# Kernel tuning notes

Measured on AMD Instinct MI355X. Metric: run time of the kernel, lower is better.

Reference implementation:

```python
import jax, jax.numpy as jnp
import numpy as np

V, E, H, B, T = 32000, 256, 512, 16, 256


def setup_inputs() -> dict:
    key = jax.random.key(0)
    ks = jax.random.split(key, 12)
    s = 1.0 / np.sqrt(H)  # torch nn.RNN init range
    u = lambda k, shape: jax.random.uniform(k, shape, jnp.float32, -s, s)
    return dict(
        X=jax.random.randint(ks[0], (B, T), 0, V),
        emb=jax.random.normal(ks[1], (V, E), jnp.float32),
        W_ih0=u(ks[2], (H, E)), W_hh0=u(ks[3], (H, H)),
        b_ih0=u(ks[4], (H,)), b_hh0=u(ks[5], (H,)),
        W_ih1=u(ks[6], (H, H)), W_hh1=u(ks[7], (H, H)),
        b_ih1=u(ks[8], (H,)), b_hh1=u(ks[9], (H,)),
        W_fc=u(ks[10], (V, H)), b_fc=u(ks[11], (V,)),
    )


def _rnn_layer(x, W_ih, W_hh, b_ih, b_hh):
    """Elman RNN layer, batch_first. x: [B,T,D] -> (outputs [B,T,H], h_T [B,H]).
    h_t = tanh(x_t @ W_ih^T + b_ih + h_{t-1} @ W_hh^T + b_hh), h_0 = 0."""
    # Precompute the input projection for all timesteps (one big GEMM).
    xp = jnp.einsum('btd,hd->bth', x, W_ih) + b_ih + b_hh  # [B,T,H]

    def step(h, xt):
        h = jnp.tanh(xt + h @ W_hh.T)
        return h, h

    h0 = jnp.zeros((x.shape[0], W_hh.shape[0]), x.dtype)
    hT, ys = jax.lax.scan(step, h0, jnp.swapaxes(xp, 0, 1))  # scan over T
    return jnp.swapaxes(ys, 0, 1), hT


def reference(X, emb, W_ih0, W_hh0, b_ih0, b_hh0,
              W_ih1, W_hh1, b_ih1, b_hh1, W_fc, b_fc):
    x = emb[X]  # [B,T,E]
    out1, h1 = _rnn_layer(x, W_ih0, W_hh0, b_ih0, b_hh0)
    out2, h2 = _rnn_layer(out1, W_ih1, W_hh1, b_ih1, b_hh1)
    logits = jnp.einsum('bth,vh->btv', out2, W_fc) + b_fc  # [B,T,V]
    hidden = jnp.stack([h1, h2], axis=0)  # [n_layers, B, H]
    return logits, hidden, out2
```

## Files before the change

kernel.cpp:

```cpp
#include <hip/hip_runtime.h>
#include <hip/hip_fp16.h>

#define BB 16
#define TT 256
#define HH 512
#define EE 256
#define VV 32000

using half8   = __attribute__((ext_vector_type(8))) _Float16;
using float4v = __attribute__((ext_vector_type(4))) float;
typedef unsigned long long u64;

#define WS_WFC16   0u
#define WS_XG      32768000u
#define WS_WIH0    34865152u
#define WS_WIH1    35127296u
#define WS_XP0     35651584u
#define WS_XP1     44040192u
#define WS_H0EX    52428800u
#define WS_OUT2F16 56623104u
#define WS_FLAGS   60817408u
#define WS_NEEDED  60833792u

__global__ void init_flags_k(unsigned* f) {
    f[blockIdx.x * 256 + threadIdx.x] = 0u;
}

__global__ void cvt_f32_f16_k(const float* __restrict__ s, _Float16* __restrict__ d, int n) {
    int i = blockIdx.x * 256 + threadIdx.x;
    if (i < n) d[i] = (_Float16)s[i];
}

__global__ void gather_embed_k(const int* __restrict__ X, const float* __restrict__ emb,
                               _Float16* __restrict__ xg) {
    int m = blockIdx.x;
    int e = threadIdx.x;
    int row = X[m];
    xg[m * EE + e] = (_Float16)emb[(size_t)row * EE + e];
}

template <bool PERM>
__global__ __launch_bounds__(256)
void gemm_f16_k(const _Float16* __restrict__ A, const _Float16* __restrict__ Bm,
                const float* __restrict__ bias0, const float* __restrict__ bias1,
                float* __restrict__ C, int M, int N, int K) {
    __shared__ _Float16 As[128][40];
    __shared__ _Float16 Bs[128][40];
    const int tid = threadIdx.x;
    const int l = tid & 63, w = tid >> 6;
    const int ntiles = N >> 7;
    const int m0 = (blockIdx.x / ntiles) << 7;
    const int n0 = (blockIdx.x % ntiles) << 7;
    const int wr = (w >> 1) << 6, wc = (w & 1) << 6;
    const int lrow = tid >> 1, lseg = (tid & 1) << 4;
    const int ar = l & 15, ak = (l >> 4) << 3;

    float4v acc[4][4] = {};

    for (int kt = 0; kt < K; kt += 32) {
        const _Float16* ga = A  + (size_t)(m0 + lrow) * K + kt + lseg;
        const _Float16* gb = Bm + (size_t)(n0 + lrow) * K + kt + lseg;
        *(int4*)&As[lrow][lseg]     = *(const int4*)ga;
        *(int4*)&As[lrow][lseg + 8] = *(const int4*)(ga + 8);
        *(int4*)&Bs[lrow][lseg]     = *(const int4*)gb;
        *(int4*)&Bs[lrow][lseg + 8] = *(const int4*)(gb + 8);
        __syncthreads();

        half8 af[4], bf[4];
#pragma unroll
        for (int m = 0; m < 4; ++m) af[m] = *(half8*)&As[wr + m * 16 + ar][ak];
#pragma unroll
        for (int n = 0; n < 4; ++n) bf[n] = *(half8*)&Bs[wc + n * 16 + ar][ak];
#pragma unroll
        for (int m = 0; m < 4; ++m)
#pragma unroll
            for (int n = 0; n < 4; ++n)
                acc[m][n] = __builtin_amdgcn_mfma_f32_16x16x32_f16(af[m], bf[n], acc[m][n], 0, 0, 0);
        __syncthreads();
    }

#pragma unroll
    for (int m = 0; m < 4; ++m) {
#pragma unroll
        for (int n = 0; n < 4; ++n) {
            const int col = n0 + wc + n * 16 + (l & 15);
            float bv = (bias0 ? bias0[col] : 0.f) + (bias1 ? bias1[col] : 0.f);
#pragma unroll
            for (int r = 0; r < 4; ++r) {
                const int row = m0 + wr + m * 16 + ((l >> 4) << 2) + r;
                float v = acc[m][n][r] + bv;
                if (PERM) {
                    int t = row & 255, b = row >> 8;
                    C[(size_t)((t << 4) + b) * HH + col] = v;
                } else {
                    C[(size_t)row * N + col] = v;
                }
            }
        }
    }
}

__device__ __forceinline__ float tanh_fast(float x) {
    float e = __expf(2.0f * x);
    return 1.0f - 2.0f * __builtin_amdgcn_rcpf(e + 1.0f);
}

__global__ __launch_bounds__(512, 2)
void rnn_pipe_k(const float* __restrict__ Whh0, const float* __restrict__ Whh1,
                const _Float16* __restrict__ Wih1f16,
                const float* __restrict__ bih1, const float* __restrict__ bhh1,
                const float* __restrict__ xp0, float* __restrict__ xp1,
                unsigned* __restrict__ h0ex,
                _Float16* __restrict__ out2f16, float* __restrict__ out_hidden,
                float* __restrict__ out2f32,
                unsigned* __restrict__ flags0, unsigned* __restrict__ flag1x)
{
    __shared__ _Float16 hbuf[16][520];
    __shared__ _Float16 wlds[8 * 4 * 4 * 64 * 8];

    const int tid = threadIdx.x;
    const int l = tid & 63, w = tid >> 6;
    const int lq = l >> 4;
    const int kq = lq << 3;
    const int c15 = l & 15;
    const int bi = blockIdx.x;

    if (bi < 2) {
        const int layer = bi;
        const float* Whh = layer ? Whh1 : Whh0;

        half8 wf[4][12];
#pragma unroll
        for (int ct = 0; ct < 4; ++ct) {
            const int col = w * 64 + ct * 16 + c15;
            const float* wrow = Whh + (size_t)col * HH;
#pragma unroll
            for (int kt = 0; kt < 16; ++kt) {
                const float* s = wrow + kt * 32 + kq;
                float4v f0 = *(const float4v*)s;
                float4v f1 = *(const float4v*)(s + 4);
                half8 h;
#pragma unroll
                for (int i = 0; i < 4; ++i) { h[i] = (_Float16)f0[i]; h[i + 4] = (_Float16)f1[i]; }
                if (kt < 12) wf[ct][kt] = h;
                else *(half8*)&wlds[((((w * 4 + ct) * 4) + (kt - 12)) * 64 + l) * 8] = h;
            }
        }

        float4v acc[4], accn[4];
        if (layer == 0) {
#pragma unroll
            for (int ct = 0; ct < 4; ++ct) {
                const int col = w * 64 + ct * 16 + c15;
#pragma unroll
                for (int r = 0; r < 4; ++r)
                    acc[ct][r] = xp0[(size_t)(lq * 4 + r) * HH + col];
            }
        } else {
            while (!__hip_atomic_load(&flag1x[0], __ATOMIC_ACQUIRE, __HIP_MEMORY_SCOPE_AGENT))
                __builtin_amdgcn_s_sleep(2);
#pragma unroll
            for (int ct = 0; ct < 4; ++ct) {
                const int col = w * 64 + ct * 16 + c15;
#pragma unroll
                for (int r = 0; r < 4; ++r)
                    acc[ct][r] = __hip_atomic_load(&xp1[(size_t)(lq * 4 + r) * HH + col],
                                                   __ATOMIC_RELAXED, __HIP_MEMORY_SCOPE_AGENT);
            }
        }
        __syncthreads();

        for (int t = 0; t < TT; ++t) {
            if (t > 0) {
#pragma unroll
                for (int kt = 0; kt < 16; ++kt) {
                    half8 a = *(const half8*)&hbuf[c15][kt * 32 + kq];
                    half8 b0, b1, b2, b3;
                    if (kt < 12) {
                        b0 = wf[0][kt]; b1 = wf[1][kt]; b2 = wf[2][kt]; b3 = wf[3][kt];
                    } else {
                        b0 = *(const half8*)&wlds[((((w * 4 + 0) * 4) + (kt - 12)) * 64 + l) * 8];
                        b1 = *(const half8*)&wlds[((((w * 4 + 1) * 4) + (kt - 12)) * 64 + l) * 8];
                        b2 = *(const half8*)&wlds[((((w * 4 + 2) * 4) + (kt - 12)) * 64 + l) * 8];
                        b3 = *(const half8*)&wlds[((((w * 4 + 3) * 4) + (kt - 12)) * 64 + l) * 8];
                    }
                    acc[0] = __builtin_amdgcn_mfma_f32_16x16x32_f16(a, b0, acc[0], 0, 0, 0);
                    acc[1] = __builtin_amdgcn_mfma_f32_16x16x32_f16(a, b1, acc[1], 0, 0, 0);
                    acc[2] = __builtin_amdgcn_mfma_f32_16x16x32_f16(a, b2, acc[2], 0, 0, 0);
                    acc[3] = __builtin_amdgcn_mfma_f32_16x16x32_f16(a, b3, acc[3], 0, 0, 0);
                }
            }

            if (layer == 0 && t > 0) {
                asm volatile("s_waitcnt vmcnt(0)" ::: "memory");
                if (l == 0)
                    __hip_atomic_store(&flags0[(t - 1) * 8 + w], 1u,
                                       __ATOMIC_RELAXED, __HIP_MEMORY_SCOPE_AGENT);
            }

            if (t + 1 < TT) {
                if (layer == 0) {
#pragma unroll
                    for (int ct = 0; ct < 4; ++ct) {
                        const int col = w * 64 + ct * 16 + c15;
#pragma unroll
                        for (int r = 0; r < 4; ++r)
                            accn[ct][r] = xp0[(size_t)((t + 1) * 16 + lq * 4 + r) * HH + col];
                    }
                } else {
                    while (!__hip_atomic_load(&flag1x[t + 1], __ATOMIC_ACQUIRE, __HIP_MEMORY_SCOPE_AGENT))
                        __builtin_amdgcn_s_sleep(2);
#pragma unroll
                    for (int ct = 0; ct < 4; ++ct) {
                        const int col = w * 64 + ct * 16 + c15;
#pragma unroll
                        for (int r = 0; r < 4; ++r)
                            accn[ct][r] = __hip_atomic_load(&xp1[(size_t)((t + 1) * 16 + lq * 4 + r) * HH + col],
                                                            __ATOMIC_RELAXED, __HIP_MEMORY_SCOPE_AGENT);
                    }
                }
            }

            unsigned pk[4][4];
#pragma unroll
            for (int ct = 0; ct < 4; ++ct) {
                const int col = w * 64 + ct * 16 + c15;
#pragma unroll
                for (int r = 0; r < 4; ++r) {
                    const int b = lq * 4 + r;
                    float hv = tanh_fast(acc[ct][r]);
                    if (layer)
                        out2f32[((size_t)(b << 8) + t) * HH + col] = hv;
                    if (t == TT - 1)
                        out_hidden[(size_t)(layer * BB + b) * HH + col] = hv;
                    unsigned short mu = __builtin_bit_cast(unsigned short, (_Float16)hv);
                    int ov = __shfl_xor((int)mu, 1, 64);
                    pk[ct][r] = (unsigned)mu | ((unsigned)ov << 16);
                }
            }

            if (layer == 0) {
                unsigned* dst = h0ex + (size_t)t * 4096;
#pragma unroll
                for (int ct = 0; ct < 4; ++ct) {
                    const int col = w * 64 + ct * 16 + c15;
#pragma unroll
                    for (int r = 0; r < 4; ++r)
                        if ((l & 1) == 0)
                            __hip_atomic_store(&dst[(lq * 4 + r) * 256 + (col >> 1)], pk[ct][r],
                                               __ATOMIC_RELAXED, __HIP_MEMORY_SCOPE_AGENT);
                }
            } else {
#pragma unroll
                for (int ct = 0; ct < 4; ++ct) {
                    const int col = w * 64 + ct * 16 + c15;
#pragma unroll
                    for (int r = 0; r < 4; ++r)
                        if ((l & 1) == 0)
                            *(unsigned*)&out2f16[((size_t)((lq * 4 + r) << 8) + t) * HH + col] = pk[ct][r];
                }
            }

            asm volatile("" ::: "memory");
            __builtin_amdgcn_s_barrier();
            asm volatile("" ::: "memory");

#pragma unroll
            for (int ct = 0; ct < 4; ++ct) {
                const int col = w * 64 + ct * 16 + c15;
#pragma unroll
                for (int r = 0; r < 4; ++r)
                    if ((l & 1) == 0)
                        *(unsigned*)&hbuf[lq * 4 + r][col] = pk[ct][r];
            }
            asm volatile("s_waitcnt lgkmcnt(0)" ::: "memory");
            __builtin_amdgcn_s_barrier();
            asm volatile("" ::: "memory");

            if (t + 1 < TT) {
#pragma unroll
                for (int ct = 0; ct < 4; ++ct) acc[ct] = accn[ct];
            }
        }

        if (layer == 0) {
            asm volatile("s_waitcnt vmcnt(0)" ::: "memory");
            if (l == 0)
                __hip_atomic_store(&flags0[(TT - 1) * 8 + w], 1u,
                                   __ATOMIC_RELAXED, __HIP_MEMORY_SCOPE_AGENT);
        }
    } else {
        const int stripe = bi - 2;
        float bsum[4];
#pragma unroll
        for (int ct = 0; ct < 4; ++ct) {
            const int col = w * 64 + ct * 16 + c15;
            bsum[ct] = bih1[col] + bhh1[col];
        }
        const int base64 = c15 * 128 + lq * 2;

        for (int j = 0; j < 8; ++j) {
            const int t = stripe + 32 * j;
            for (;;) {
                unsigned v = 1u;
                if (l < 8)
                    v = __hip_atomic_load(&flags0[t * 8 + l], __ATOMIC_ACQUIRE, __HIP_MEMORY_SCOPE_AGENT);
                if (__all(v != 0)) break;
                __builtin_amdgcn_s_sleep(2);
            }
            half8 af[16];
            const u64* pA = (const u64*)h0ex + (size_t)t * 2048;
#pragma unroll
            for (int kt = 0; kt < 16; ++kt) {
                u64 d0 = __hip_atomic_load(pA + base64 + kt * 8,     __ATOMIC_RELAXED, __HIP_MEMORY_SCOPE_AGENT);
                u64 d1 = __hip_atomic_load(pA + base64 + kt * 8 + 1, __ATOMIC_RELAXED, __HIP_MEMORY_SCOPE_AGENT);
                union { u64 u[2]; half8 h; } cv;
                cv.u[0] = d0; cv.u[1] = d1;
                af[kt] = cv.h;
            }
            float4v acc[4];
#pragma unroll
            for (int ct = 0; ct < 4; ++ct) {
                acc[ct][0] = bsum[ct]; acc[ct][1] = bsum[ct];
                acc[ct][2] = bsum[ct]; acc[ct][3] = bsum[ct];
            }
#pragma unroll
            for (int ct = 0; ct < 4; ++ct) {
                const int col = w * 64 + ct * 16 + c15;
                const _Float16* wp = Wih1f16 + (size_t)col * HH + kq;
#pragma unroll
                for (int kt = 0; kt < 16; ++kt) {
                    half8 bf = *(const half8*)(wp + kt * 32);
                    acc[ct] = __builtin_amdgcn_mfma_f32_16x16x32_f16(af[kt], bf, acc[ct], 0, 0, 0);
                }
            }
#pragma unroll
            for (int ct = 0; ct < 4; ++ct) {
                const int col = w * 64 + ct * 16 + c15;
#pragma unroll
                for (int r = 0; r < 4; ++r)
                    __hip_atomic_store(&xp1[(size_t)(t * 16 + lq * 4 + r) * HH + col], acc[ct][r],
                                       __ATOMIC_RELAXED, __HIP_MEMORY_SCOPE_AGENT);
            }
            __syncthreads();
            if (tid == 0)
                __hip_atomic_store(&flag1x[t], 1u, __ATOMIC_RELEASE, __HIP_MEMORY_SCOPE_AGENT);
        }
    }
}

extern "C" void kernel_launch(void* const* d_in, const int* in_sizes, int n_in,
                              void* d_out, int out_size, void* d_ws, size_t ws_size,
                              hipStream_t stream) {
    if (ws_size < WS_NEEDED) return;

    const int*   X     = (const int*)d_in[0];
    const float* emb   = (const float*)d_in[1];
    const float* Wih0  = (const float*)d_in[2];
    const float* Whh0  = (const float*)d_in[3];
    const float* bih0  = (const float*)d_in[4];
    const float* bhh0  = (const float*)d_in[5];
    const float* Wih1  = (const float*)d_in[6];
    const float* Whh1  = (const float*)d_in[7];
    const float* bih1  = (const float*)d_in[8];
    const float* bhh1  = (const float*)d_in[9];
    const float* Wfc   = (const float*)d_in[10];
    const float* bfc   = (const float*)d_in[11];

    char* ws = (char*)d_ws;
    _Float16* Wfc16   = (_Float16*)(ws + WS_WFC16);
    _Float16* xg      = (_Float16*)(ws + WS_XG);
    _Float16* Wih0f16 = (_Float16*)(ws + WS_WIH0);
    _Float16* Wih1f16 = (_Float16*)(ws + WS_WIH1);
    float*    xp0     = (float*)(ws + WS_XP0);
    float*    xp1     = (float*)(ws + WS_XP1);
    unsigned* h0ex    = (unsigned*)(ws + WS_H0EX);
    _Float16* o2f16   = (_Float16*)(ws + WS_OUT2F16);
    unsigned* flags0  = (unsigned*)(ws + WS_FLAGS);
    unsigned* flag1x  = flags0 + TT * 8;

    float* logits     = (float*)d_out;
    float* hidden     = (float*)d_out + (size_t)BB * TT * VV;
    float* out2       = hidden + 2 * BB * HH;

    hipLaunchKernelGGL(init_flags_k, dim3(9), dim3(256), 0, stream, flags0);
    hipLaunchKernelGGL(gather_embed_k, dim3(BB * TT), dim3(256), 0, stream, X, emb, xg);
    hipLaunchKernelGGL(cvt_f32_f16_k, dim3((HH * EE) / 256), dim3(256), 0, stream, Wih0, Wih0f16, HH * EE);
    hipLaunchKernelGGL(cvt_f32_f16_k, dim3((HH * HH) / 256), dim3(256), 0, stream, Wih1, Wih1f16, HH * HH);
    hipLaunchKernelGGL(cvt_f32_f16_k, dim3((VV * HH) / 256), dim3(256), 0, stream, Wfc, Wfc16, VV * HH);

    hipLaunchKernelGGL((gemm_f16_k<true>), dim3((4096 / 128) * (HH / 128)), dim3(256), 0, stream,
                       xg, Wih0f16, bih0, bhh0, xp0, 4096, HH, EE);

    hipLaunchKernelGGL(rnn_pipe_k, dim3(34), dim3(512), 0, stream,
                       Whh0, Whh1, Wih1f16, bih1, bhh1, xp0, xp1,
                       h0ex, o2f16, hidden, out2, flags0, flag1x);

    hipLaunchKernelGGL((gemm_f16_k<false>), dim3((4096 / 128) * (VV / 128)), dim3(256), 0, stream,
                       o2f16, Wfc16, bfc, nullptr, logits, 4096, VV, HH);
}
```

Baseline: 1.989 ms.

## Halve recurrent block to 4 waves with 128 columns each, restructure step pipeline

Cuts the recurrent blocks from 8 to 4 wavefronts, so each wave owns 128 hidden columns. That doubles the register-held W_hh fragments and the per-wave MFMA count, while the LDS-resident part shrinks to 4 k-tiles. The input projection is no longer prefetched into a second accumulator; it is loaded mid-step between the two MFMA halves and added before tanh. Layer 1 peeks its flag at the start of the step and only spins after the first MFMAs. The aim is to cut barrier and sync overhead per timestep and hide load latency behind the matmul, at the cost of more register pressure and fewer waves sharing the serial step.

Result: slower. 2.361 ms (+18.7%).

```diff
diff --git a/kernel.cpp b/kernel.cpp
--- a/kernel.cpp
+++ b/kernel.cpp
@@ -105,7 +105,7 @@
     return 1.0f - 2.0f * __builtin_amdgcn_rcpf(e + 1.0f);
 }
 
-__global__ __launch_bounds__(512, 2)
+__global__ __launch_bounds__(256, 1)
 void rnn_pipe_k(const float* __restrict__ Whh0, const float* __restrict__ Whh1,
                 const _Float16* __restrict__ Wih1f16,
                 const float* __restrict__ bih1, const float* __restrict__ bhh1,
@@ -116,7 +116,7 @@
                 unsigned* __restrict__ flags0, unsigned* __restrict__ flag1x)
 {
     __shared__ _Float16 hbuf[16][520];
-    __shared__ _Float16 wlds[8 * 4 * 4 * 64 * 8];
+    __shared__ _Float16 wlds[4 * 8 * 4 * 64 * 8];
 
     const int tid = threadIdx.x;
     const int l = tid & 63, w = tid >> 6;
@@ -129,10 +129,10 @@
         const int layer = bi;
         const float* Whh = layer ? Whh1 : Whh0;
 
-        half8 wf[4][12];
-#pragma unroll
-        for (int ct = 0; ct < 4; ++ct) {
-            const int col = w * 64 + ct * 16 + c15;
+        half8 wf[8][12];
+#pragma unroll
+        for (int ct = 0; ct < 8; ++ct) {
+            const int col = w * 128 + ct * 16 + c15;
             const float* wrow = Whh + (size_t)col * HH;
 #pragma unroll
             for (int kt = 0; kt < 16; ++kt) {
@@ -142,93 +142,92 @@
                 half8 h;
 #pragma unroll
                 for (int i = 0; i < 4; ++i) { h[i] = (_Float16)f0[i]; h[i + 4] = (_Float16)f1[i]; }
-                if (kt < 12) wf[ct][kt] = h;
-                else *(half8*)&wlds[((((w * 4 + ct) * 4) + (kt - 12)) * 64 + l) * 8] = h;
-            }
-        }
-
-        float4v acc[4], accn[4];
-        if (layer == 0) {
-#pragma unroll
-            for (int ct = 0; ct < 4; ++ct) {
-                const int col = w * 64 + ct * 16 + c15;
-#pragma unroll
-                for (int r = 0; r < 4; ++r)
-                    acc[ct][r] = xp0[(size_t)(lq * 4 + r) * HH + col];
-            }
-        } else {
-            while (!__hip_atomic_load(&flag1x[0], __ATOMIC_ACQUIRE, __HIP_MEMORY_SCOPE_AGENT))
-                __builtin_amdgcn_s_sleep(2);
-#pragma unroll
-            for (int ct = 0; ct < 4; ++ct) {
-                const int col = w * 64 + ct * 16 + c15;
-#pragma unroll
-                for (int r = 0; r < 4; ++r)
-                    acc[ct][r] = __hip_atomic_load(&xp1[(size_t)(lq * 4 + r) * HH + col],
-                                                   __ATOMIC_RELAXED, __HIP_MEMORY_SCOPE_AGENT);
+                if (kt < 4) *(half8*)&wlds[((((w * 8 + ct) * 4) + kt) * 64 + l) * 8] = h;
+                else wf[ct][kt - 4] = h;
             }
         }
         __syncthreads();
 
+        float4v acc[8] = {};
         for (int t = 0; t < TT; ++t) {
+            unsigned fpre = 1u;
+            if (layer == 0) {
+                if (t > 0) {
+                    asm volatile("s_waitcnt vmcnt(0)" ::: "memory");
+                    if (l == 0)
+                        __hip_atomic_store(&flags0[(t - 1) * 4 + w], 1u,
+                                           __ATOMIC_RELAXED, __HIP_MEMORY_SCOPE_AGENT);
+                }
+            } else {
+                fpre = __hip_atomic_load(&flag1x[t], __ATOMIC_RELAXED, __HIP_MEMORY_SCOPE_AGENT);
+            }
+
             if (t > 0) {
 #pragma unroll
-                for (int kt = 0; kt < 16; ++kt) {
+                for (int kt = 0; kt < 4; ++kt) {
                     half8 a = *(const half8*)&hbuf[c15][kt * 32 + kq];
-                    half8 b0, b1, b2, b3;
-                    if (kt < 12) {
-                        b0 = wf[0][kt]; b1 = wf[1][kt]; b2 = wf[2][kt]; b3 = wf[3][kt];
-                    } else {
-                        b0 = *(const half8*)&wlds[((((w * 4 + 0) * 4) + (kt - 12)) * 64 + l) * 8];
-                        b1 = *(const half8*)&wlds[((((w * 4 + 1) * 4) + (kt - 12)) * 64 + l) * 8];
-                        b2 = *(const half8*)&wlds[((((w * 4 + 2) * 4) + (kt - 12)) * 64 + l) * 8];
-                        b3 = *(const half8*)&wlds[((((w * 4 + 3) * 4) + (kt - 12)) * 64 + l) * 8];
+#pragma unroll
+                    for (int ct = 0; ct < 8; ++ct) {
+                        half8 b = *(const half8*)&wlds[((((w * 8 + ct) * 4) + kt) * 64 + l) * 8];
+                        acc[ct] = __builtin_amdgcn_mfma_f32_16x16x32_f16(a, b, acc[ct], 0, 0, 0);
                     }
-                    acc[0] = __builtin_amdgcn_mfma_f32_16x16x32_f16(a, b0, acc[0], 0, 0, 0);
-                    acc[1] = __builtin_amdgcn_mfma_f32_16x16x32_f16(a, b1, acc[1], 0, 0, 0);
-                    acc[2] = __builtin_amdgcn_mfma_f32_16x16x32_f16(a, b2, acc[2], 0, 0, 0);
-                    acc[3] = __builtin_amdgcn_mfma_f32_16x16x32_f16(a, b3, acc[3], 0, 0, 0);
-                }
-            }
-
-            if (layer == 0 && t > 0) {
-                asm volatile("s_waitcnt vmcnt(0)" ::: "memory");
-                if (l == 0)
-                    __hip_atomic_store(&flags0[(t - 1) * 8 + w], 1u,
-                                       __ATOMIC_RELAXED, __HIP_MEMORY_SCOPE_AGENT);
-            }
-
-            if (t + 1 < TT) {
-                if (layer == 0) {
-#pragma unroll
-                    for (int ct = 0; ct < 4; ++ct) {
-                        const int col = w * 64 + ct * 16 + c15;
-#pragma unroll
-                        for (int r = 0; r < 4; ++r)
-                            accn[ct][r] = xp0[(size_t)((t + 1) * 16 + lq * 4 + r) * HH + col];
-                    }
+                }
+#pragma unroll
+                for (int kt = 4; kt < 8; ++kt) {
+                    half8 a = *(const half8*)&hbuf[c15][kt * 32 + kq];
+#pragma unroll
+                    for (int ct = 0; ct < 8; ++ct)
+                        acc[ct] = __builtin_amdgcn_mfma_f32_16x16x32_f16(a, wf[ct][kt - 4], acc[ct], 0, 0, 0);
+                }
+            }
+
+            if (layer == 1) {
+                if (fpre) {
+                    __builtin_amdgcn_fence(__ATOMIC_ACQUIRE, "agent");
                 } else {
-                    while (!__hip_atomic_load(&flag1x[t + 1], __ATOMIC_ACQUIRE, __HIP_MEMORY_SCOPE_AGENT))
+                    while (!__hip_atomic_load(&flag1x[t], __ATOMIC_ACQUIRE, __HIP_MEMORY_SCOPE_AGENT))
                         __builtin_amdgcn_s_sleep(2);
-#pragma unroll
-                    for (int ct = 0; ct < 4; ++ct) {
-                        const int col = w * 64 + ct * 16 + c15;
-#pragma unroll
-                        for (int r = 0; r < 4; ++r)
-                            accn[ct][r] = __hip_atomic_load(&xp1[(size_t)((t + 1) * 16 + lq * 4 + r) * HH + col],
-                                                            __ATOMIC_RELAXED, __HIP_MEMORY_SCOPE_AGENT);
-                    }
-                }
-            }
-
-            unsigned pk[4][4];
-#pragma unroll
-            for (int ct = 0; ct < 4; ++ct) {
-                const int col = w * 64 + ct * 16 + c15;
+                }
+            }
+
+            float xv[8][4];
+            if (layer == 0) {
+#pragma unroll
+                for (int ct = 0; ct < 8; ++ct) {
+                    const int col = w * 128 + ct * 16 + c15;
+#pragma unroll
+                    for (int r = 0; r < 4; ++r)
+                        xv[ct][r] = xp0[(size_t)(t * 16 + lq * 4 + r) * HH + col];
+                }
+            } else {
+#pragma unroll
+                for (int ct = 0; ct < 8; ++ct) {
+                    const int col = w * 128 + ct * 16 + c15;
+#pragma unroll
+                    for (int r = 0; r < 4; ++r)
+                        xv[ct][r] = __hip_atomic_load(&xp1[(size_t)(t * 16 + lq * 4 + r) * HH + col],
+                                                      __ATOMIC_RELAXED, __HIP_MEMORY_SCOPE_AGENT);
+                }
+            }
+
+            if (t > 0) {
+#pragma unroll
+                for (int kt = 8; kt < 16; ++kt) {
+                    half8 a = *(const half8*)&hbuf[c15][kt * 32 + kq];
+#pragma unroll
+                    for (int ct = 0; ct < 8; ++ct)
+                        acc[ct] = __builtin_amdgcn_mfma_f32_16x16x32_f16(a, wf[ct][kt - 4], acc[ct], 0, 0, 0);
+                }
+            }
+
+            unsigned pk[8][4];
+#pragma unroll
+            for (int ct = 0; ct < 8; ++ct) {
+                const int col = w * 128 + ct * 16 + c15;
 #pragma unroll
                 for (int r = 0; r < 4; ++r) {
                     const int b = lq * 4 + r;
-                    float hv = tanh_fast(acc[ct][r]);
+                    float hv = tanh_fast(xv[ct][r] + acc[ct][r]);
                     if (layer)
                         out2f32[((size_t)(b << 8) + t) * HH + col] = hv;
                     if (t == TT - 1)
@@ -236,14 +235,15 @@
                     unsigned short mu = __builtin_bit_cast(unsigned short, (_Float16)hv);
                     int ov = __shfl_xor((int)mu, 1, 64);
                     pk[ct][r] = (unsigned)mu | ((unsigned)ov << 16);
+                    acc[ct][r] = 0.f;
                 }
             }
 
             if (layer == 0) {
                 unsigned* dst = h0ex + (size_t)t * 4096;
 #pragma unroll
-                for (int ct = 0; ct < 4; ++ct) {
-                    const int col = w * 64 + ct * 16 + c15;
+                for (int ct = 0; ct < 8; ++ct) {
+                    const int col = w * 128 + ct * 16 + c15;
 #pragma unroll
                     for (int r = 0; r < 4; ++r)
                         if ((l & 1) == 0)
@@ -252,8 +252,8 @@
                 }
             } else {
 #pragma unroll
-                for (int ct = 0; ct < 4; ++ct) {
-                    const int col = w * 64 + ct * 16 + c15;
+                for (int ct = 0; ct < 8; ++ct) {
+                    const int col = w * 128 + ct * 16 + c15;
 #pragma unroll
                     for (int r = 0; r < 4; ++r)
                         if ((l & 1) == 0)
@@ -266,8 +266,8 @@
             asm volatile("" ::: "memory");
 
 #pragma unroll
-            for (int ct = 0; ct < 4; ++ct) {
-                const int col = w * 64 + ct * 16 + c15;
+            for (int ct = 0; ct < 8; ++ct) {
+                const int col = w * 128 + ct * 16 + c15;
 #pragma unroll
                 for (int r = 0; r < 4; ++r)
                     if ((l & 1) == 0)
@@ -276,25 +276,20 @@
             asm volatile("s_waitcnt lgkmcnt(0)" ::: "memory");
             __builtin_amdgcn_s_barrier();
             asm volatile("" ::: "memory");
-
-            if (t + 1 < TT) {
-#pragma unroll
-                for (int ct = 0; ct < 4; ++ct) acc[ct] = accn[ct];
-            }
         }
 
         if (layer == 0) {
             asm volatile("s_waitcnt vmcnt(0)" ::: "memory");
             if (l == 0)
-                __hip_atomic_store(&flags0[(TT - 1) * 8 + w], 1u,
+                __hip_atomic_store(&flags0[(TT - 1) * 4 + w], 1u,
                                    __ATOMIC_RELAXED, __HIP_MEMORY_SCOPE_AGENT);
         }
     } else {
         const int stripe = bi - 2;
-        float bsum[4];
-#pragma unroll
-        for (int ct = 0; ct < 4; ++ct) {
-            const int col = w * 64 + ct * 16 + c15;
+        float bsum[8];
+#pragma unroll
+        for (int ct = 0; ct < 8; ++ct) {
+            const int col = w * 128 + ct * 16 + c15;
             bsum[ct] = bih1[col] + bhh1[col];
         }
         const int base64 = c15 * 128 + lq * 2;
@@ -303,8 +298,8 @@
             const int t = stripe + 32 * j;
             for (;;) {
                 unsigned v = 1u;
-                if (l < 8)
-                    v = __hip_atomic_load(&flags0[t * 8 + l], __ATOMIC_ACQUIRE, __HIP_MEMORY_SCOPE_AGENT);
+                if (l < 4)
+                    v = __hip_atomic_load(&flags0[t * 4 + l], __ATOMIC_ACQUIRE, __HIP_MEMORY_SCOPE_AGENT);
                 if (__all(v != 0)) break;
                 __builtin_amdgcn_s_sleep(2);
             }
@@ -318,15 +313,15 @@
                 cv.u[0] = d0; cv.u[1] = d1;
                 af[kt] = cv.h;
             }
-            float4v acc[4];
-#pragma unroll
-            for (int ct = 0; ct < 4; ++ct) {
+            float4v acc[8];
+#pragma unroll
+            for (int ct = 0; ct < 8; ++ct) {
                 acc[ct][0] = bsum[ct]; acc[ct][1] = bsum[ct];
                 acc[ct][2] = bsum[ct]; acc[ct][3] = bsum[ct];
             }
 #pragma unroll
-            for (int ct = 0; ct < 4; ++ct) {
-                const int col = w * 64 + ct * 16 + c15;
+            for (int ct = 0; ct < 8; ++ct) {
+                const int col = w * 128 + ct * 16 + c15;
                 const _Float16* wp = Wih1f16 + (size_t)col * HH + kq;
 #pragma unroll
                 for (int kt = 0; kt < 16; ++kt) {
@@ -335,8 +330,8 @@
                 }
             }
 #pragma unroll
-            for (int ct = 0; ct < 4; ++ct) {
-                const int col = w * 64 + ct * 16 + c15;
+            for (int ct = 0; ct < 8; ++ct) {
+                const int col = w * 128 + ct * 16 + c15;
 #pragma unroll
                 for (int r = 0; r < 4; ++r)
                     __hip_atomic_store(&xp1[(size_t)(t * 16 + lq * 4 + r) * HH + col], acc[ct][r],
@@ -377,7 +372,7 @@
     unsigned* h0ex    = (unsigned*)(ws + WS_H0EX);
     _Float16* o2f16   = (_Float16*)(ws + WS_OUT2F16);
     unsigned* flags0  = (unsigned*)(ws + WS_FLAGS);
-    unsigned* flag1x  = flags0 + TT * 8;
+    unsigned* flag1x  = flags0 + TT * 4;
 
     float* logits     = (float*)d_out;
     float* hidden     = (float*)d_out + (size_t)BB * TT * VV;
@@ -392,7 +387,7 @@
     hipLaunchKernelGGL((gemm_f16_k<true>), dim3((4096 / 128) * (HH / 128)), dim3(256), 0, stream,
                        xg, Wih0f16, bih0, bhh0, xp0, 4096, HH, EE);
 
-    hipLaunchKernelGGL(rnn_pipe_k, dim3(34), dim3(512), 0, stream,
+    hipLaunchKernelGGL(rnn_pipe_k, dim3(34), dim3(256), 0, stream,
                        Whh0, Whh1, Wih1f16, bih1, bhh1, xp0, xp1,
                        h0ex, o2f16, hidden, out2, flags0, flag1x);
 
```

## Split each RNN layer's recurrence across two workgroups with flag-based hidden-state exchange

Applied to the files above, without the earlier changes.

Each recurrent layer now runs on two 256-thread workgroups that each own half of the hidden columns. They exchange half-precision hidden states every timestep through global memory and per-step flags. Because each wave now holds all 16 K-tiles of its W_hh slice in registers, the LDS-resident weight part is removed. The layer-1 input projection is split into 64 column-stripe workgroups signalled by per-stripe flags. The output GEMM reads layer-1 hidden states from the exchange buffer with a permuted row index, so the separate out2 f16 copy is no longer written. This shortens per-step MFMA chains, but adds a cross-workgroup handshake on the serial critical path of every step.

New measurement: 3.092 ms. 55.4% more time.

```diff
diff --git a/kernel.cpp b/kernel.cpp
--- a/kernel.cpp
+++ b/kernel.cpp
@@ -18,7 +18,7 @@
 #define WS_XP0     35651584u
 #define WS_XP1     44040192u
 #define WS_H0EX    52428800u
-#define WS_OUT2F16 56623104u
+#define WS_H1EX    56623104u
 #define WS_FLAGS   60817408u
 #define WS_NEEDED  60833792u
 
@@ -39,7 +39,7 @@
     xg[m * EE + e] = (_Float16)emb[(size_t)row * EE + e];
 }
 
-template <bool PERM>
+template <bool PERM, bool APERM>
 __global__ __launch_bounds__(256)
 void gemm_f16_k(const _Float16* __restrict__ A, const _Float16* __restrict__ Bm,
                 const float* __restrict__ bias0, const float* __restrict__ bias1,
@@ -57,8 +57,11 @@
 
     float4v acc[4][4] = {};
 
+    const int am = m0 + lrow;
+    const size_t arow = APERM ? (size_t)((am & 255) * 16 + (am >> 8)) : (size_t)am;
+
     for (int kt = 0; kt < K; kt += 32) {
-        const _Float16* ga = A  + (size_t)(m0 + lrow) * K + kt + lseg;
+        const _Float16* ga = A  + arow * K + kt + lseg;
         const _Float16* gb = Bm + (size_t)(n0 + lrow) * K + kt + lseg;
         *(int4*)&As[lrow][lseg]     = *(const int4*)ga;
         *(int4*)&As[lrow][lseg + 8] = *(const int4*)(ga + 8);
@@ -105,18 +108,17 @@
     return 1.0f - 2.0f * __builtin_amdgcn_rcpf(e + 1.0f);
 }
 
-__global__ __launch_bounds__(512, 2)
+__global__ __launch_bounds__(256, 1)
 void rnn_pipe_k(const float* __restrict__ Whh0, const float* __restrict__ Whh1,
                 const _Float16* __restrict__ Wih1f16,
                 const float* __restrict__ bih1, const float* __restrict__ bhh1,
                 const float* __restrict__ xp0, float* __restrict__ xp1,
-                unsigned* __restrict__ h0ex,
-                _Float16* __restrict__ out2f16, float* __restrict__ out_hidden,
-                float* __restrict__ out2f32,
-                unsigned* __restrict__ flags0, unsigned* __restrict__ flag1x)
+                unsigned* __restrict__ h0ex, unsigned* __restrict__ h1ex,
+                float* __restrict__ out_hidden, float* __restrict__ out2f32,
+                unsigned* __restrict__ flags0, unsigned* __restrict__ flags1,
+                unsigned* __restrict__ flagsS)
 {
     __shared__ _Float16 hbuf[16][520];
-    __shared__ _Float16 wlds[8 * 4 * 4 * 64 * 8];
 
     const int tid = threadIdx.x;
     const int l = tid & 63, w = tid >> 6;
@@ -125,15 +127,23 @@
     const int c15 = l & 15;
     const int bi = blockIdx.x;
 
-    if (bi < 2) {
-        const int layer = bi;
+    if (bi < 4) {
+        const int layer = bi >> 1, p = bi & 1;
         const float* Whh = layer ? Whh1 : Whh0;
-
-        half8 wf[4][12];
+        const int rk = (1 - p) * 256;
+        unsigned* myfl = layer ? flags1 : flags0;
+        unsigned* pfl  = myfl;
+        unsigned* hex  = layer ? h1ex : h0ex;
+        const u64* rex = (const u64*)hex;
+
+        int col[4];
+#pragma unroll
+        for (int ct = 0; ct < 4; ++ct) col[ct] = p * 256 + w * 64 + ct * 16 + c15;
+
+        half8 wf[4][16];
 #pragma unroll
         for (int ct = 0; ct < 4; ++ct) {
-            const int col = w * 64 + ct * 16 + c15;
-            const float* wrow = Whh + (size_t)col * HH;
+            const float* wrow = Whh + (size_t)col[ct] * HH;
 #pragma unroll
             for (int kt = 0; kt < 16; ++kt) {
                 const float* s = wrow + kt * 32 + kq;
@@ -142,209 +152,179 @@
                 half8 h;
 #pragma unroll
                 for (int i = 0; i < 4; ++i) { h[i] = (_Float16)f0[i]; h[i + 4] = (_Float16)f1[i]; }
-                if (kt < 12) wf[ct][kt] = h;
-                else *(half8*)&wlds[((((w * 4 + ct) * 4) + (kt - 12)) * 64 + l) * 8] = h;
+                wf[ct][kt] = h;
             }
         }
-
-        float4v acc[4], accn[4];
-        if (layer == 0) {
-#pragma unroll
-            for (int ct = 0; ct < 4; ++ct) {
-                const int col = w * 64 + ct * 16 + c15;
-#pragma unroll
-                for (int r = 0; r < 4; ++r)
-                    acc[ct][r] = xp0[(size_t)(lq * 4 + r) * HH + col];
-            }
-        } else {
-            while (!__hip_atomic_load(&flag1x[0], __ATOMIC_ACQUIRE, __HIP_MEMORY_SCOPE_AGENT))
-                __builtin_amdgcn_s_sleep(2);
-#pragma unroll
-            for (int ct = 0; ct < 4; ++ct) {
-                const int col = w * 64 + ct * 16 + c15;
-#pragma unroll
-                for (int r = 0; r < 4; ++r)
-                    acc[ct][r] = __hip_atomic_load(&xp1[(size_t)(lq * 4 + r) * HH + col],
-                                                   __ATOMIC_RELAXED, __HIP_MEMORY_SCOPE_AGENT);
-            }
-        }
-        __syncthreads();
 
         for (int t = 0; t < TT; ++t) {
             if (t > 0) {
+                asm volatile("s_waitcnt vmcnt(0)" ::: "memory");
+                asm volatile("" ::: "memory");
+                __builtin_amdgcn_s_barrier();
+                asm volatile("" ::: "memory");
+                if (tid == 0)
+                    __hip_atomic_store(&myfl[(t - 1) * 2 + p], 1u,
+                                       __ATOMIC_RELEASE, __HIP_MEMORY_SCOPE_AGENT);
+            }
+
+            if (w == 0) {
+                for (;;) {
+                    unsigned v = 1u;
+                    if (layer == 0) {
+                        if (t > 0 && l == 0)
+                            v = __hip_atomic_load(&pfl[(t - 1) * 2 + (1 - p)],
+                                                  __ATOMIC_ACQUIRE, __HIP_MEMORY_SCOPE_AGENT);
+                    } else {
+                        if (t > 0 && l == 0)
+                            v = __hip_atomic_load(&pfl[(t - 1) * 2 + (1 - p)],
+                                                  __ATOMIC_ACQUIRE, __HIP_MEMORY_SCOPE_AGENT);
+                        else if (l >= 4 && l < 8)
+                            v = __hip_atomic_load(&flagsS[t * 8 + p * 4 + (l - 4)],
+                                                  __ATOMIC_ACQUIRE, __HIP_MEMORY_SCOPE_AGENT);
+                    }
+                    if (__all(v != 0)) break;
+                    __builtin_amdgcn_s_sleep(4);
+                }
+            }
+            __syncthreads();
+
+            if (t > 0) {
+#pragma unroll
+                for (int j = 0; j < 4; ++j) {
+                    int idx = j * 256 + tid;
+                    int b = idx >> 6, q = idx & 63;
+                    u64 d = __hip_atomic_load(rex + ((size_t)(t - 1) * 16 + b) * 128 + (rk >> 2) + q,
+                                              __ATOMIC_RELAXED, __HIP_MEMORY_SCOPE_AGENT);
+                    *(u64*)&hbuf[b][rk + q * 4] = d;
+                }
+            }
+            float4v acc[4];
+#pragma unroll
+            for (int ct = 0; ct < 4; ++ct) {
+#pragma unroll
+                for (int r = 0; r < 4; ++r) {
+                    if (layer == 0)
+                        acc[ct][r] = xp0[(size_t)(t * 16 + lq * 4 + r) * HH + col[ct]];
+                    else
+                        acc[ct][r] = __hip_atomic_load(&xp1[(size_t)(t * 16 + lq * 4 + r) * HH + col[ct]],
+                                                       __ATOMIC_RELAXED, __HIP_MEMORY_SCOPE_AGENT);
+                }
+            }
+
+            if (t > 0) {
+                asm volatile("s_waitcnt lgkmcnt(0)" ::: "memory");
+                __builtin_amdgcn_s_barrier();
+                asm volatile("" ::: "memory");
+
 #pragma unroll
                 for (int kt = 0; kt < 16; ++kt) {
                     half8 a = *(const half8*)&hbuf[c15][kt * 32 + kq];
-                    half8 b0, b1, b2, b3;
-                    if (kt < 12) {
-                        b0 = wf[0][kt]; b1 = wf[1][kt]; b2 = wf[2][kt]; b3 = wf[3][kt];
-                    } else {
-                        b0 = *(const half8*)&wlds[((((w * 4 + 0) * 4) + (kt - 12)) * 64 + l) * 8];
-                        b1 = *(const half8*)&wlds[((((w * 4 + 1) * 4) + (kt - 12)) * 64 + l) * 8];
-                        b2 = *(const half8*)&wlds[((((w * 4 + 2) * 4) + (kt - 12)) * 64 + l) * 8];
-                        b3 = *(const half8*)&wlds[((((w * 4 + 3) * 4) + (kt - 12)) * 64 + l) * 8];
-                    }
-                    acc[0] = __builtin_amdgcn_mfma_f32_16x16x32_f16(a, b0, acc[0], 0, 0, 0);
-                    acc[1] = __builtin_amdgcn_mfma_f32_16x16x32_f16(a, b1, acc[1], 0, 0, 0);
-                    acc[2] = __builtin_amdgcn_mfma_f32_16x16x32_f16(a, b2, acc[2], 0, 0, 0);
-                    acc[3] = __builtin_amdgcn_mfma_f32_16x16x32_f16(a, b3, acc[3], 0, 0, 0);
-                }
-            }
-
-            if (layer == 0 && t > 0) {
-                asm volatile("s_waitcnt vmcnt(0)" ::: "memory");
-                if (l == 0)
-                    __hip_atomic_store(&flags0[(t - 1) * 8 + w], 1u,
-                                       __ATOMIC_RELAXED, __HIP_MEMORY_SCOPE_AGENT);
-            }
-
-            if (t + 1 < TT) {
-                if (layer == 0) {
-#pragma unroll
-                    for (int ct = 0; ct < 4; ++ct) {
-                        const int col = w * 64 + ct * 16 + c15;
-#pragma unroll
-                        for (int r = 0; r < 4; ++r)
-                            accn[ct][r] = xp0[(size_t)((t + 1) * 16 + lq * 4 + r) * HH + col];
-                    }
-                } else {
-                    while (!__hip_atomic_load(&flag1x[t + 1], __ATOMIC_ACQUIRE, __HIP_MEMORY_SCOPE_AGENT))
-                        __builtin_amdgcn_s_sleep(2);
-#pragma unroll
-                    for (int ct = 0; ct < 4; ++ct) {
-                        const int col = w * 64 + ct * 16 + c15;
-#pragma unroll
-                        for (int r = 0; r < 4; ++r)
-                            accn[ct][r] = __hip_atomic_load(&xp1[(size_t)((t + 1) * 16 + lq * 4 + r) * HH + col],
-                                                            __ATOMIC_RELAXED, __HIP_MEMORY_SCOPE_AGENT);
-                    }
+                    acc[0] = __builtin_amdgcn_mfma_f32_16x16x32_f16(a, wf[0][kt], acc[0], 0, 0, 0);
+                    acc[1] = __builtin_amdgcn_mfma_f32_16x16x32_f16(a, wf[1][kt], acc[1], 0, 0, 0);
+                    acc[2] = __builtin_amdgcn_mfma_f32_16x16x32_f16(a, wf[2][kt], acc[2], 0, 0, 0);
+                    acc[3] = __builtin_amdgcn_mfma_f32_16x16x32_f16(a, wf[3][kt], acc[3], 0, 0, 0);
                 }
             }
 
             unsigned pk[4][4];
 #pragma unroll
             for (int ct = 0; ct < 4; ++ct) {
-                const int col = w * 64 + ct * 16 + c15;
 #pragma unroll
                 for (int r = 0; r < 4; ++r) {
                     const int b = lq * 4 + r;
                     float hv = tanh_fast(acc[ct][r]);
-                    if (layer)
-                        out2f32[((size_t)(b << 8) + t) * HH + col] = hv;
+                    if (layer == 1)
+                        out2f32[((size_t)(b << 8) + t) * HH + col[ct]] = hv;
                     if (t == TT - 1)
-                        out_hidden[(size_t)(layer * BB + b) * HH + col] = hv;
+                        out_hidden[(size_t)(layer * BB + b) * HH + col[ct]] = hv;
                     unsigned short mu = __builtin_bit_cast(unsigned short, (_Float16)hv);
                     int ov = __shfl_xor((int)mu, 1, 64);
                     pk[ct][r] = (unsigned)mu | ((unsigned)ov << 16);
                 }
             }
 
-            if (layer == 0) {
-                unsigned* dst = h0ex + (size_t)t * 4096;
+            if ((l & 1) == 0) {
 #pragma unroll
                 for (int ct = 0; ct < 4; ++ct) {
-                    const int col = w * 64 + ct * 16 + c15;
-#pragma unroll
-                    for (int r = 0; r < 4; ++r)
-                        if ((l & 1) == 0)
-                            __hip_atomic_store(&dst[(lq * 4 + r) * 256 + (col >> 1)], pk[ct][r],
-                                               __ATOMIC_RELAXED, __HIP_MEMORY_SCOPE_AGENT);
-                }
-            } else {
-#pragma unroll
-                for (int ct = 0; ct < 4; ++ct) {
-                    const int col = w * 64 + ct * 16 + c15;
-#pragma unroll
-                    for (int r = 0; r < 4; ++r)
-                        if ((l & 1) == 0)
-                            *(unsigned*)&out2f16[((size_t)((lq * 4 + r) << 8) + t) * HH + col] = pk[ct][r];
+#pragma unroll
+                    for (int r = 0; r < 4; ++r) {
+                        const int b = lq * 4 + r;
+                        __hip_atomic_store(&hex[((size_t)t * 16 + b) * 256 + (col[ct] >> 1)], pk[ct][r],
+                                           __ATOMIC_RELAXED, __HIP_MEMORY_SCOPE_AGENT);
+                    }
                 }
             }
 
             asm volatile("" ::: "memory");
             __builtin_amdgcn_s_barrier();
             asm volatile("" ::: "memory");
-
-#pragma unroll
-            for (int ct = 0; ct < 4; ++ct) {
-                const int col = w * 64 + ct * 16 + c15;
-#pragma unroll
-                for (int r = 0; r < 4; ++r)
-                    if ((l & 1) == 0)
-                        *(unsigned*)&hbuf[lq * 4 + r][col] = pk[ct][r];
-            }
-            asm volatile("s_waitcnt lgkmcnt(0)" ::: "memory");
-            __builtin_amdgcn_s_barrier();
-            asm volatile("" ::: "memory");
-
-            if (t + 1 < TT) {
-#pragma unroll
-                for (int ct = 0; ct < 4; ++ct) acc[ct] = accn[ct];
+            if ((l & 1) == 0) {
+#pragma unroll
+                for (int ct = 0; ct < 4; ++ct) {
+#pragma unroll
+                    for (int r = 0; r < 4; ++r)
+                        *(unsigned*)&hbuf[lq * 4 + r][col[ct]] = pk[ct][r];
+                }
             }
         }
 
-        if (layer == 0) {
-            asm volatile("s_waitcnt vmcnt(0)" ::: "memory");
-            if (l == 0)
-                __hip_atomic_store(&flags0[(TT - 1) * 8 + w], 1u,
-                                   __ATOMIC_RELAXED, __HIP_MEMORY_SCOPE_AGENT);
-        }
+        asm volatile("s_waitcnt vmcnt(0)" ::: "memory");
+        asm volatile("" ::: "memory");
+        __builtin_amdgcn_s_barrier();
+        asm volatile("" ::: "memory");
+        if (tid == 0)
+            __hip_atomic_store(&myfl[(TT - 1) * 2 + p], 1u,
+                               __ATOMIC_RELEASE, __HIP_MEMORY_SCOPE_AGENT);
     } else {
-        const int stripe = bi - 2;
-        float bsum[4];
-#pragma unroll
-        for (int ct = 0; ct < 4; ++ct) {
-            const int col = w * 64 + ct * 16 + c15;
-            bsum[ct] = bih1[col] + bhh1[col];
-        }
-        const int base64 = c15 * 128 + lq * 2;
-
-        for (int j = 0; j < 8; ++j) {
-            const int t = stripe + 32 * j;
-            for (;;) {
-                unsigned v = 1u;
-                if (l < 8)
-                    v = __hip_atomic_load(&flags0[t * 8 + l], __ATOMIC_ACQUIRE, __HIP_MEMORY_SCOPE_AGENT);
-                if (__all(v != 0)) break;
-                __builtin_amdgcn_s_sleep(2);
-            }
+        const int sb = bi - 4;
+        const int cs = sb & 7;
+        const int j  = sb >> 3;
+        const int col = cs * 64 + w * 16 + c15;
+
+        half8 wfi[16];
+#pragma unroll
+        for (int kt = 0; kt < 16; ++kt)
+            wfi[kt] = *(const half8*)(Wih1f16 + (size_t)col * HH + kt * 32 + kq);
+        const float bsum = bih1[col] + bhh1[col];
+
+        const u64* hx = (const u64*)h0ex;
+
+        for (int t = j; t < TT; t += 8) {
+            if (w == 0) {
+                for (;;) {
+                    unsigned v = 1u;
+                    if (l < 2)
+                        v = __hip_atomic_load(&flags0[t * 2 + l],
+                                              __ATOMIC_ACQUIRE, __HIP_MEMORY_SCOPE_AGENT);
+                    if (__all(v != 0)) break;
+                    __builtin_amdgcn_s_sleep(16);
+                }
+            }
+            __syncthreads();
+
             half8 af[16];
-            const u64* pA = (const u64*)h0ex + (size_t)t * 2048;
+            const size_t rb = ((size_t)t * 16 + c15) * 128 + (kq >> 2);
 #pragma unroll
             for (int kt = 0; kt < 16; ++kt) {
-                u64 d0 = __hip_atomic_load(pA + base64 + kt * 8,     __ATOMIC_RELAXED, __HIP_MEMORY_SCOPE_AGENT);
-                u64 d1 = __hip_atomic_load(pA + base64 + kt * 8 + 1, __ATOMIC_RELAXED, __HIP_MEMORY_SCOPE_AGENT);
+                u64 d0 = __hip_atomic_load(hx + rb + kt * 8,     __ATOMIC_RELAXED, __HIP_MEMORY_SCOPE_AGENT);
+                u64 d1 = __hip_atomic_load(hx + rb + kt * 8 + 1, __ATOMIC_RELAXED, __HIP_MEMORY_SCOPE_AGENT);
                 union { u64 u[2]; half8 h; } cv;
                 cv.u[0] = d0; cv.u[1] = d1;
                 af[kt] = cv.h;
             }
-            float4v acc[4];
-#pragma unroll
-            for (int ct = 0; ct < 4; ++ct) {
-                acc[ct][0] = bsum[ct]; acc[ct][1] = bsum[ct];
-                acc[ct][2] = bsum[ct]; acc[ct][3] = bsum[ct];
-            }
-#pragma unroll
-            for (int ct = 0; ct < 4; ++ct) {
-                const int col = w * 64 + ct * 16 + c15;
-                const _Float16* wp = Wih1f16 + (size_t)col * HH + kq;
-#pragma unroll
-                for (int kt = 0; kt < 16; ++kt) {
-                    half8 bf = *(const half8*)(wp + kt * 32);
-                    acc[ct] = __builtin_amdgcn_mfma_f32_16x16x32_f16(af[kt], bf, acc[ct], 0, 0, 0);
-                }
-            }
-#pragma unroll
-            for (int ct = 0; ct < 4; ++ct) {
-                const int col = w * 64 + ct * 16 + c15;
-#pragma unroll
-                for (int r = 0; r < 4; ++r)
-                    __hip_atomic_store(&xp1[(size_t)(t * 16 + lq * 4 + r) * HH + col], acc[ct][r],
-                                       __ATOMIC_RELAXED, __HIP_MEMORY_SCOPE_AGENT);
-            }
+            float4v acc = {bsum, bsum, bsum, bsum};
+#pragma unroll
+            for (int kt = 0; kt < 16; ++kt)
+                acc = __builtin_amdgcn_mfma_f32_16x16x32_f16(af[kt], wfi[kt], acc, 0, 0, 0);
+
+#pragma unroll
+            for (int r = 0; r < 4; ++r)
+                __hip_atomic_store(&xp1[(size_t)(t * 16 + lq * 4 + r) * HH + col], acc[r],
+                                   __ATOMIC_RELAXED, __HIP_MEMORY_SCOPE_AGENT);
             __syncthreads();
             if (tid == 0)
-                __hip_atomic_store(&flag1x[t], 1u, __ATOMIC_RELEASE, __HIP_MEMORY_SCOPE_AGENT);
+                __hip_atomic_store(&flagsS[t * 8 + cs], 1u,
+                                   __ATOMIC_RELEASE, __HIP_MEMORY_SCOPE_AGENT);
         }
     }
 }
@@ -375,27 +355,28 @@
     float*    xp0     = (float*)(ws + WS_XP0);
     float*    xp1     = (float*)(ws + WS_XP1);
     unsigned* h0ex    = (unsigned*)(ws + WS_H0EX);
-    _Float16* o2f16   = (_Float16*)(ws + WS_OUT2F16);
+    unsigned* h1ex    = (unsigned*)(ws + WS_H1EX);
     unsigned* flags0  = (unsigned*)(ws + WS_FLAGS);
-    unsigned* flag1x  = flags0 + TT * 8;
+    unsigned* flags1  = flags0 + 512;
+    unsigned* flagsS  = flags0 + 1024;
 
     float* logits     = (float*)d_out;
     float* hidden     = (float*)d_out + (size_t)BB * TT * VV;
     float* out2       = hidden + 2 * BB * HH;
 
-    hipLaunchKernelGGL(init_flags_k, dim3(9), dim3(256), 0, stream, flags0);
+    hipLaunchKernelGGL(init_flags_k, dim3(12), dim3(256), 0, stream, flags0);
     hipLaunchKernelGGL(gather_embed_k, dim3(BB * TT), dim3(256), 0, stream, X, emb, xg);
     hipLaunchKernelGGL(cvt_f32_f16_k, dim3((HH * EE) / 256), dim3(256), 0, stream, Wih0, Wih0f16, HH * EE);
     hipLaunchKernelGGL(cvt_f32_f16_k, dim3((HH * HH) / 256), dim3(256), 0, stream, Wih1, Wih1f16, HH * HH);
     hipLaunchKernelGGL(cvt_f32_f16_k, dim3((VV * HH) / 256), dim3(256), 0, stream, Wfc, Wfc16, VV * HH);
 
-    hipLaunchKernelGGL((gemm_f16_k<true>), dim3((4096 / 128) * (HH / 128)), dim3(256), 0, stream,
+    hipLaunchKernelGGL((gemm_f16_k<true, false>), dim3((4096 / 128) * (HH / 128)), dim3(256), 0, stream,
                        xg, Wih0f16, bih0, bhh0, xp0, 4096, HH, EE);
 
-    hipLaunchKernelGGL(rnn_pipe_k, dim3(34), dim3(512), 0, stream,
+    hipLaunchKernelGGL(rnn_pipe_k, dim3(68), dim3(256), 0, stream,
                        Whh0, Whh1, Wih1f16, bih1, bhh1, xp0, xp1,
-                       h0ex, o2f16, hidden, out2, flags0, flag1x);
-
-    hipLaunchKernelGGL((gemm_f16_k<false>), dim3((4096 / 128) * (VV / 128)), dim3(256), 0, stream,
-                       o2f16, Wfc16, bfc, nullptr, logits, 4096, VV, HH);
-}
+                       h0ex, h1ex, hidden, out2, flags0, flags1, flagsS);
+
+    hipLaunchKernelGGL((gemm_f16_k<false, true>), dim3((4096 / 128) * (VV / 128)), dim3(256), 0, stream,
+                       (const _Float16*)h1ex, Wfc16, bfc, nullptr, logits, 4096, VV, HH);
+}
```
